# Kernel optimization log

Measured on AMD Instinct MI355X. Metric: run time of the kernel, lower is better.

Reference implementation:

```python
import jax, jax.numpy as jnp
import numpy as np

B, C_IN, H, W = 8, 64, 128, 128
NUM_POINT = 128
N_INST = 512
INIT_STRIDE, COARSE_STRIDE, DOWN_SAMPLE = 10.0, 4.0, 4.0
D_MODEL, N_HEADS = 256, 8


def conv2d(x, w, b, pad):
    y = jax.lax.conv_general_dilated(x, w, (1, 1), [(pad, pad), (pad, pad)],
                                     dimension_numbers=('NCHW', 'OIHW', 'NCHW'))
    return y + b[None, :, None, None]


def trans_feature(x, w1, b1, w2, b2):
    # Conv3x3 -> ReLU -> Conv1x1 (c_in -> 256 -> 254)
    return conv2d(jax.nn.relu(conv2d(x, w1, b1, 1)), w2, b2, 0)


def grid_sample_points(feat, img_idx, pts):
    # get_gcn_feature: per-instance bilinear sampling of feat[img_idx] at pixel
    # coords pts. torch grid_sample(align_corners=False, padding_mode='zeros');
    # the normalize->unnormalize of pixel coords collapses to a -0.5 shift.
    Bf, C, Hf, Wf = feat.shape
    ix = pts[..., 0] - 0.5
    iy = pts[..., 1] - 0.5
    x0 = jnp.floor(ix)
    y0 = jnp.floor(iy)
    wx = ix - x0
    wy = iy - y0

    def gather(yy, xx, wgt):
        valid = (xx >= 0) & (xx < Wf) & (yy >= 0) & (yy < Hf)
        xc = jnp.clip(xx, 0, Wf - 1).astype(jnp.int32)
        yc = jnp.clip(yy, 0, Hf - 1).astype(jnp.int32)
        v = feat[img_idx[:, None], :, yc, xc]  # [N,P,C]
        return v * (wgt * valid)[..., None]

    return (gather(y0, x0, (1 - wx) * (1 - wy)) + gather(y0, x0 + 1, wx * (1 - wy))
            + gather(y0 + 1, x0, (1 - wx) * wy) + gather(y0 + 1, x0 + 1, wx * wy))


def normalize_poly(poly):
    # Center each contour and scale by its max extent -> positional encoding in [-1,1]
    mean = poly.mean(axis=1, keepdims=True)
    p = poly - mean
    scale = jnp.max(jnp.abs(p), axis=(1, 2), keepdims=True) + 1e-6
    return p / scale


def csa(x, wqkv, bqkv, wo, bo, whead, bhead):
    # ContourSelfAttention: MHSA over contour points + linear head to 2D offsets
    N, P, C = x.shape
    d = C // N_HEADS
    qkv = x @ wqkv + bqkv
    q, k, v = jnp.split(qkv, 3, axis=-1)
    sh = lambda t: t.reshape(N, P, N_HEADS, d).transpose(0, 2, 1, 3)
    q, k, v = sh(q), sh(k), sh(v)
    attn = jax.nn.softmax(jnp.einsum('nhpd,nhqd->nhpq', q, k) / jnp.sqrt(jnp.float32(d)), axis=-1)
    o = jnp.einsum('nhpq,nhqd->nhpd', attn, v).transpose(0, 2, 1, 3).reshape(N, P, C)
    o = o @ wo + bo
    return o @ whead + bhead  # [N,P,2]


def setup_inputs():
    key = jax.random.key(0)
    ks = jax.random.split(key, 32)
    s = 0.05
    inp = {
        'cnn_feature': jax.random.normal(ks[0], (B, C_IN, H, W), jnp.float32),
        'wh_pred': jax.random.normal(ks[1], (B, 2 * NUM_POINT, H, W), jnp.float32),
        'ct_ind': jax.random.randint(ks[2], (N_INST,), 0, H * W),
        'ct_img_idx': jax.random.randint(ks[3], (N_INST,), 0, B),
    }
    p = lambda i, shape: jax.random.normal(ks[i], shape, jnp.float32) * s
    for pre, i0 in (('f1', 4), ('f2', 8)):
        inp[pre + '_w1'] = p(i0, (256, C_IN, 3, 3))
        inp[pre + '_b1'] = p(i0 + 1, (256,))
        inp[pre + '_w2'] = p(i0 + 2, (254, 256, 1, 1))
        inp[pre + '_b2'] = p(i0 + 3, (254,))
    for pre, i0 in (('csa1', 12), ('csa2', 18)):
        inp[pre + '_wqkv'] = p(i0, (D_MODEL, 3 * D_MODEL))
        inp[pre + '_bqkv'] = p(i0 + 1, (3 * D_MODEL,))
        inp[pre + '_wo'] = p(i0 + 2, (D_MODEL, D_MODEL))
        inp[pre + '_bo'] = p(i0 + 3, (D_MODEL,))
        inp[pre + '_whead'] = p(i0 + 4, (D_MODEL, 2))
        inp[pre + '_bhead'] = p(i0 + 5, (2,))
    return inp


def reference(cnn_feature, wh_pred, ct_ind, ct_img_idx,
              f1_w1, f1_b1, f1_w2, f1_b2, f2_w1, f2_b1, f2_w2, f2_b2,
              csa1_wqkv, csa1_bqkv, csa1_wo, csa1_bo, csa1_whead, csa1_bhead,
              csa2_wqkv, csa2_bqkv, csa2_wo, csa2_bo, csa2_whead, csa2_bhead):
    # ---- Decode.train_decode ----
    ct_x = ct_ind % W
    ct_y = ct_ind // W
    # per-instance gather of contour offsets: wh_pred[img, :, y, x] -> [N, 2*P]
    ct_offset = wh_pred[ct_img_idx, :, ct_y, ct_x].reshape(-1, NUM_POINT, 2)
    ct = jnp.stack([ct_x, ct_y], axis=1).astype(jnp.float32)  # [N,2]
    init_polys = ct_offset * INIT_STRIDE + ct[:, None, :]     # [N,128,2]
    # ---- Refine ----
    feat1 = trans_feature(cnn_feature, f1_w1, f1_b1, f1_w2, f1_b2)  # [B,254,H,W]
    feat2 = trans_feature(cnn_feature, f2_w1, f2_b1, f2_w2, f2_b2)
    points = jnp.concatenate([ct[:, None, :], init_polys], axis=1)  # [N,129,2]
    fp1 = grid_sample_points(feat1, ct_img_idx, points)             # [N,129,254]
    x1 = jnp.concatenate([fp1, normalize_poly(points)], axis=-1)    # [N,129,256]
    offsets1 = csa(x1, csa1_wqkv, csa1_bqkv, csa1_wo, csa1_bo, csa1_whead, csa1_bhead)[:, 1:, :]
    coarse_polys = offsets1 * COARSE_STRIDE + jax.lax.stop_gradient(init_polys)
    fp2 = grid_sample_points(feat2, ct_img_idx, coarse_polys)       # [N,128,254]
    x2 = jnp.concatenate([fp2, normalize_poly(coarse_polys)], axis=-1)
    offsets2 = csa(x2, csa2_wqkv, csa2_bqkv, csa2_wo, csa2_bo, csa2_whead, csa2_bhead)
    final_polys = offsets2 + jax.lax.stop_gradient(coarse_polys)
    return (init_polys * DOWN_SAMPLE, coarse_polys * DOWN_SAMPLE, final_polys * DOWN_SAMPLE)
```

## Files before the change

kernel.cpp:

```cpp
#include <hip/hip_runtime.h>
#include <hip/hip_bf16.h>

typedef unsigned short u16;
typedef unsigned int   u32;
typedef float  f32x4 __attribute__((ext_vector_type(4)));
typedef short  s16x8 __attribute__((ext_vector_type(8)));

__device__ __forceinline__ float bf2f(u16 u) {
    return __uint_as_float(((unsigned int)u) << 16);
}
__device__ __forceinline__ u16 f2bf(float f) {
    unsigned int x = __float_as_uint(f);
    unsigned int r = x + 0x7fffu + ((x >> 16) & 1u);
    return (u16)(r >> 16);
}

#define WIMG 128
#define HIMG 128
#define PADW 130
#define BIMG 8
#define CIN  64
#define NPOINT 128
#define NINST 512

#define AS1 __attribute__((address_space(1)))
#define AS3 __attribute__((address_space(3)))
__device__ __forceinline__ void async16(const void* g, void* l) {
    __builtin_amdgcn_global_load_lds((const AS1 void*)g, (AS3 void*)l, 16, 0, 0);
}

__global__ __launch_bounds__(256) void k_cvt_w1(const float* __restrict__ w,
                                                u16* __restrict__ wb) {
    int idx = blockIdx.x * 256 + threadIdx.x;
    int oc = idx / 576, r = idx % 576;
    int kp = r >> 6, ic = r & 63;
    wb[idx] = f2bf(w[oc * 576 + ic * 9 + kp]);
}

__global__ __launch_bounds__(256) void k_cvt_w2(const float* __restrict__ w,
                                                u16* __restrict__ wb) {
    int idx = blockIdx.x * 256 + threadIdx.x;
    int oc = idx >> 8, ic = idx & 255;
    wb[idx] = (oc < 254) ? f2bf(w[oc * 256 + ic]) : (u16)0;
}

__global__ __launch_bounds__(256) void k_cvt_wqkv(const float* __restrict__ w,
                                                  u16* __restrict__ wb) {
    int idx = blockIdx.x * 256 + threadIdx.x;
    int n = idx >> 8, k = idx & 255;
    wb[idx] = f2bf(w[k * 768 + n]);
}

__global__ __launch_bounds__(256) void k_headfuse(const float* __restrict__ wo,
                                                  const float* __restrict__ bo,
                                                  const float* __restrict__ whead,
                                                  const float* __restrict__ bhead,
                                                  float* __restrict__ W2,
                                                  float* __restrict__ b2) {
    int idx = blockIdx.x * 256 + threadIdx.x;
    if (idx < 512) {
        int c = idx >> 1, j = idx & 1;
        float s = 0.f;
        for (int t = 0; t < 256; ++t)
            s = fmaf(wo[c * 256 + t], whead[t * 2 + j], s);
        W2[idx] = s;
    }
    if (idx < 2) {
        float s = bhead[idx];
        for (int t = 0; t < 256; ++t)
            s = fmaf(bo[t], whead[t * 2 + idx], s);
        b2[idx] = s;
    }
}

__global__ __launch_bounds__(256) void k_zero(u16* __restrict__ p) {
    int i = blockIdx.x * 256 + threadIdx.x;
    ((uint4*)p)[i] = make_uint4(0u, 0u, 0u, 0u);
}

__global__ __launch_bounds__(256) void k_nhwc(const float* __restrict__ in,
                                              u16* __restrict__ out) {
    __shared__ u16 sT[128][80];
    int b = blockIdx.x >> 7, y = blockIdx.x & 127;
    int tid = threadIdx.x;
    const float* ib = in + ((size_t)b * CIN * HIMG + y) * WIMG;
    int x4 = tid & 31, icg = tid >> 5;
    #pragma unroll
    for (int pass = 0; pass < 8; ++pass) {
        int ic = pass * 8 + icg;
        float4 v = *(const float4*)&ib[(size_t)ic * (HIMG * WIMG) + x4 * 4];
        sT[x4 * 4 + 0][ic] = f2bf(v.x);
        sT[x4 * 4 + 1][ic] = f2bf(v.y);
        sT[x4 * 4 + 2][ic] = f2bf(v.z);
        sT[x4 * 4 + 3][ic] = f2bf(v.w);
    }
    __syncthreads();
    u16* ob = out + ((size_t)(b * PADW + y + 1) * PADW + 1) * 64;
    int icu = tid & 7, xw = tid >> 3;
    #pragma unroll
    for (int pass = 0; pass < 4; ++pass) {
        int x = pass * 32 + xw;
        uint4 v = *(const uint4*)&sT[x][icu * 8];
        *(uint4*)&ob[(size_t)x * 64 + icu * 8] = v;
    }
}

__global__ __launch_bounds__(256) void k_init(const float* __restrict__ whp,
                                              const int* __restrict__ ct_ind,
                                              const int* __restrict__ ct_img,
                                              float* __restrict__ points1,
                                              float* __restrict__ out0) {
    int i = blockIdx.x;
    int t = threadIdx.x;
    int ind = ct_ind[i];
    int x = ind % WIMG, y = ind / WIMG;
    int b = ct_img[i];
    int p = t >> 1, c = t & 1;
    float off = whp[(((size_t)b * 2 * NPOINT + t) * HIMG + y) * WIMG + x];
    float ctc = (c == 0) ? (float)x : (float)y;
    float ip = off * 10.0f + ctc;
    points1[((size_t)i * 129 + 1 + p) * 2 + c] = ip;
    if (t < 2) points1[(size_t)i * 129 * 2 + t] = (t == 0) ? (float)x : (float)y;
    out0[((size_t)i * NPOINT + p) * 2 + c] = ip * 4.0f;
}

__global__ __launch_bounds__(256, 2) void k_convgemm(const u16* __restrict__ inTp,
                                                     const u16* __restrict__ wb1,
                                                     const float* __restrict__ b1,
                                                     const u16* __restrict__ wb2,
                                                     const float* __restrict__ b2,
                                                     u16* __restrict__ feat) {
    __shared__ u16 smem[33280];
    u16* sB = smem;
    u16* sW = smem + 16384;
    u16* sC = smem + 16384;

    int tid = threadIdx.x;
    int wave = tid >> 6, lane = tid & 63;
    int quad = lane >> 4, l16 = lane & 15;
    int rl = lane >> 2, part = lane & 3;
    int partS = part ^ ((rl ^ (rl >> 2)) & 3);
    int quadS = quad ^ ((l16 ^ (l16 >> 2)) & 3);

    int bx = blockIdx.x;
    int y = (bx & 7) * 16 + (bx >> 4);
    int half = (bx >> 3) & 1;
    int xb = half * 64;
    int b = blockIdx.z;
    const u16* inb = inTp + (size_t)b * PADW * PADW * 64;

    for (int idx = tid; idx < 1584; idx += 256) {
        int r = idx / 528, g = idx - r * 528;
        int pxw = g >> 3, c = g & 7;
        uint4 v = *(const uint4*)&inb[((size_t)(y + r) * PADW + xb + pxw) * 64 + c * 8];
        *(uint4*)&sW[((r * 66 + pxw) * 8 + (c ^ (pxw & 7))) * 8] = v;
    }

    auto stageB1 = [&](u16* dst, int t) {
        int kp = t >> 1, ic0 = (t & 1) << 5;
        const u16* brow = wb1 + (size_t)kp * 64 + ic0 + partS * 8;
        #pragma unroll
        for (int j = 0; j < 4; ++j) {
            int rr = wave * 64 + j * 16;
            async16(brow + (size_t)(rr + rl) * 576, dst + rr * 32);
        }
    };
    auto stageB2 = [&](u16* dst, int kk) {
        #pragma unroll
        for (int j = 0; j < 4; ++j) {
            int rr = wave * 64 + j * 16;
            async16(wb2 + (size_t)(rr + rl) * 256 + kk + partS * 8, dst + rr * 32);
        }
    };

    f32x4 acc1[4][4];
    #pragma unroll
    for (int mt = 0; mt < 4; ++mt)
        #pragma unroll
        for (int nt = 0; nt < 4; ++nt)
            #pragma unroll
            for (int q = 0; q < 4; ++q) acc1[mt][nt][q] = 0.f;

    stageB1(sB, 0);
    __syncthreads();
    int buf = 0;
    for (int t = 0; t < 18; ++t) {
        if (t < 17) stageB1(sB + (buf ^ 1) * 8192, t + 1);
        int kp = t >> 1, cdb = (t & 1) << 2;
        int ky = kp / 3, kx = kp - ky * 3;
        s16x8 aF[4], bF[4];
        #pragma unroll
        for (int mt = 0; mt < 4; ++mt) {
            int pxw = kx + mt * 16 + l16;
            int cd = cdb + quad;
            aF[mt] = *(const s16x8*)&sW[((ky * 66 + pxw) * 8 + (cd ^ (pxw & 7))) * 8];
        }
        #pragma unroll
        for (int nt = 0; nt < 4; ++nt)
            bF[nt] = *(const s16x8*)&sB[buf * 8192 + (wave * 64 + nt * 16 + l16) * 32 + quadS * 8];
        #pragma unroll
        for (int mt = 0; mt < 4; ++mt)
            #pragma unroll
            for (int nt = 0; nt < 4; ++nt)
                acc1[mt][nt] = __builtin_amdgcn_mfma_f32_16x16x32_bf16(
                    aF[mt], bF[nt], acc1[mt][nt], 0, 0, 0);
        __syncthreads();
        buf ^= 1;
    }

    #pragma unroll
    for (int nt = 0; nt < 4; ++nt) {
        int col = wave * 64 + nt * 16 + l16;
        float bv = b1[col];
        #pragma unroll
        for (int mt = 0; mt < 4; ++mt) {
            #pragma unroll
            for (int r = 0; r < 4; ++r) {
                int row = mt * 16 + quad * 4 + r;
                sC[row * 264 + col] = f2bf(fmaxf(acc1[mt][nt][r] + bv, 0.f));
            }
        }
    }
    stageB2(sB, 0);
    __syncthreads();

    f32x4 acc2[4][4];
    #pragma unroll
    for (int mt = 0; mt < 4; ++mt)
        #pragma unroll
        for (int nt = 0; nt < 4; ++nt)
            #pragma unroll
            for (int q = 0; q < 4; ++q) acc2[mt][nt][q] = 0.f;
    int b2f = 0;
    for (int ik = 0; ik < 8; ++ik) {
        if (ik < 7) stageB2(sB + (b2f ^ 1) * 8192, (ik + 1) * 32);
        s16x8 a2[4], bb[4];
        #pragma unroll
        for (int mt = 0; mt < 4; ++mt)
            a2[mt] = *(const s16x8*)&sC[(mt * 16 + l16) * 264 + ik * 32 + quad * 8];
        #pragma unroll
        for (int nt = 0; nt < 4; ++nt)
            bb[nt] = *(const s16x8*)&sB[b2f * 8192 + (wave * 64 + nt * 16 + l16) * 32 + quadS * 8];
        #pragma unroll
        for (int mt = 0; mt < 4; ++mt)
            #pragma unroll
            for (int nt = 0; nt < 4; ++nt)
                acc2[mt][nt] = __builtin_amdgcn_mfma_f32_16x16x32_bf16(
                    a2[mt], bb[nt], acc2[mt][nt], 0, 0, 0);
        __syncthreads();
        b2f ^= 1;
    }

    #pragma unroll
    for (int nt = 0; nt < 4; ++nt) {
        int col = wave * 64 + nt * 16 + l16;
        float bv = (col < 254) ? b2[col] : 0.f;
        #pragma unroll
        for (int mt = 0; mt < 4; ++mt) {
            #pragma unroll
            for (int r = 0; r < 4; ++r) {
                int row = mt * 16 + quad * 4 + r;
                sC[row * 264 + col] = f2bf(acc2[mt][nt][r] + bv);
            }
        }
    }
    __syncthreads();
    u16* outb = feat + ((size_t)b * (HIMG * WIMG) + (size_t)y * 128 + half * 64) * 256;
    #pragma unroll
    for (int it = 0; it < 8; ++it) {
        int idx = it * 256 + tid;
        int row = idx >> 5, ch = idx & 31;
        *(uint4*)&outb[(size_t)row * 256 + ch * 8] = *(const uint4*)&sC[row * 264 + ch * 8];
    }
}

__global__ __launch_bounds__(256, 4) void k_gemm_mfma(const u16* __restrict__ A,
                                                      const u16* __restrict__ Bt,
                                                      const float* __restrict__ bias, int nbias,
                                                      u16* __restrict__ C,
                                                      int M, int N, int K, int relu) {
    __shared__ u16 smem[16384];
    u16* sA = smem;
    u16* sB = smem + 8192;
    u16* sOut = smem;
    int tid = threadIdx.x;
    int wave = tid >> 6, lane = tid & 63;
    int quad = lane >> 4, l16 = lane & 15;
    int rl = lane >> 2, part = lane & 3;
    int partS = part ^ ((rl ^ (rl >> 2)) & 3);
    int quadS = quad ^ ((l16 ^ (l16 >> 2)) & 3);
    int r0 = wave * 32;

    int gx = gridDim.x, gy = gridDim.y;
    int o = blockIdx.y * gx + blockIdx.x;
    int nwg = gx * gy;
    int qn = nwg >> 3, r8 = nwg & 7;
    int xcd = o & 7, oi = o >> 3;
    int vid = (xcd < r8) ? xcd * (qn + 1) + oi : r8 * (qn + 1) + (xcd - r8) * qn + oi;
    int m0 = (vid / gy) * 128, n0 = (vid % gy) * 128;
    int wm = (wave >> 1) * 64, wn = (wave & 1) * 64;

    f32x4 acc[4][4];
    #pragma unroll
    for (int a = 0; a < 4; ++a)
        #pragma unroll
        for (int b = 0; b < 4; ++b)
            #pragma unroll
            for (int q = 0; q < 4; ++q) acc[a][b][q] = 0.f;

    auto stage = [&](int bufi, int kk) {
        #pragma unroll
        for (int j = 0; j < 2; ++j) {
            int rr = r0 + j * 16;
            async16(&A[(size_t)(m0 + rr + rl) * K + kk + partS * 8], &sA[bufi * 4096 + rr * 32]);
            async16(&Bt[(size_t)(n0 + rr + rl) * K + kk + partS * 8], &sB[bufi * 4096 + rr * 32]);
        }
    };

    stage(0, 0);
    __syncthreads();
    int buf = 0;
    int nk = K >> 5;
    for (int ik = 0; ik < nk; ++ik) {
        if (ik + 1 < nk) stage(buf ^ 1, (ik + 1) << 5);
        s16x8 aF[4], bF[4];
        #pragma unroll
        for (int mt = 0; mt < 4; ++mt)
            aF[mt] = *(const s16x8*)&sA[buf * 4096 + (wm + mt * 16 + l16) * 32 + quadS * 8];
        #pragma unroll
        for (int nt = 0; nt < 4; ++nt)
            bF[nt] = *(const s16x8*)&sB[buf * 4096 + (wn + nt * 16 + l16) * 32 + quadS * 8];
        #pragma unroll
        for (int mt = 0; mt < 4; ++mt)
            #pragma unroll
            for (int nt = 0; nt < 4; ++nt)
                acc[mt][nt] = __builtin_amdgcn_mfma_f32_16x16x32_bf16(
                    aF[mt], bF[nt], acc[mt][nt], 0, 0, 0);
        __syncthreads();
        buf ^= 1;
    }

    #pragma unroll
    for (int pass = 0; pass < 2; ++pass) {
        if ((wave >> 1) == pass) {
            #pragma unroll
            for (int nt = 0; nt < 4; ++nt) {
                int col = wn + nt * 16 + l16;
                int gcol = n0 + col;
                float bv = (gcol < nbias) ? bias[gcol] : 0.f;
                #pragma unroll
                for (int mt = 0; mt < 4; ++mt) {
                    #pragma unroll
                    for (int r = 0; r < 4; ++r) {
                        int rowl = mt * 16 + quad * 4 + r;
                        float v = acc[mt][nt][r] + bv;
                        if (relu) v = fmaxf(v, 0.f);
                        sOut[rowl * 132 + col] = f2bf(v);
                    }
                }
            }
        }
        __syncthreads();
        #pragma unroll
        for (int it = 0; it < 8; ++it) {
            int idx = it * 256 + tid;
            int rowl = idx >> 5, ch = idx & 31;
            *(uint2*)&C[(size_t)(m0 + pass * 64 + rowl) * N + n0 + ch * 4] =
                *(const uint2*)&sOut[rowl * 132 + ch * 4];
        }
        __syncthreads();
    }
}

__global__ __launch_bounds__(256) void k_norm(const float* __restrict__ pts,
                                              u16* __restrict__ xout, int P) {
    int i = blockIdx.x, t = threadIdx.x;
    __shared__ float sx[256], sy[256];
    float px = 0.f, py = 0.f;
    if (t < P) {
        px = pts[((size_t)i * P + t) * 2 + 0];
        py = pts[((size_t)i * P + t) * 2 + 1];
    }
    sx[t] = px; sy[t] = py;
    __syncthreads();
    for (int s = 128; s > 0; s >>= 1) {
        if (t < s) { sx[t] += sx[t + s]; sy[t] += sy[t + s]; }
        __syncthreads();
    }
    float mx = sx[0] / (float)P, my = sy[0] / (float)P;
    __syncthreads();
    float ax = 0.f;
    if (t < P) ax = fmaxf(fabsf(px - mx), fabsf(py - my));
    sx[t] = ax;
    __syncthreads();
    for (int s = 128; s > 0; s >>= 1) {
        if (t < s) sx[t] = fmaxf(sx[t], sx[t + s]);
        __syncthreads();
    }
    float scale = sx[0] + 1e-6f;
    if (t < P) {
        size_t base = ((size_t)i * P + t) * 256;
        xout[base + 254] = f2bf((px - mx) / scale);
        xout[base + 255] = f2bf((py - my) / scale);
    }
}

__global__ __launch_bounds__(256) void k_sample(const u16* __restrict__ feat,
                                                const float* __restrict__ pts,
                                                const int* __restrict__ ct_img,
                                                u16* __restrict__ xout, int P) {
    int i = blockIdx.x;
    int p = blockIdx.y * 2 + (threadIdx.x >> 7);
    int c0 = (threadIdx.x & 127) * 2;
    if (p >= P || c0 >= 254) return;
    float px = pts[((size_t)i * P + p) * 2 + 0];
    float py = pts[((size_t)i * P + p) * 2 + 1];
    int b = ct_img[i];
    float ix = px - 0.5f, iy = py - 0.5f;
    float x0f = floorf(ix), y0f = floorf(iy);
    float wx = ix - x0f, wy = iy - y0f;
    int x0 = (int)x0f, y0 = (int)y0f;
    float a0 = 0.f, a1 = 0.f;
    #pragma unroll
    for (int dy = 0; dy < 2; ++dy) {
        #pragma unroll
        for (int dx = 0; dx < 2; ++dx) {
            int xx = x0 + dx, yy = y0 + dy;
            float w = (dx ? wx : 1.f - wx) * (dy ? wy : 1.f - wy);
            if (xx >= 0 && xx < WIMG && yy >= 0 && yy < HIMG) {
                u32 v = *(const u32*)&feat[(((size_t)b * HIMG + yy) * WIMG + xx) * 256 + c0];
                a0 = fmaf(w, bf2f((u16)(v & 0xffffu)), a0);
                a1 = fmaf(w, bf2f((u16)(v >> 16)), a1);
            }
        }
    }
    u32 st = (u32)f2bf(a0) | ((u32)f2bf(a1) << 16);
    *(u32*)&xout[((size_t)i * P + p) * 256 + c0] = st;
}

__global__ __launch_bounds__(256) void k_attn_mfma(const u16* __restrict__ qkv,
                                                   u16* __restrict__ obuf,
                                                   int P) {
    __shared__ u16 smem[144 * 40 * 2 + 32 * 168];
    u16* sQ = smem;
    u16* sK = smem + 144 * 40;
    u16* sVT = smem + 2 * 144 * 40;

    int il = blockIdx.x, h = blockIdx.y;
    int tid = threadIdx.x;
    int wave = tid >> 6, lane = tid & 63;
    int quad = lane >> 4, l16 = lane & 15;

    {
        u32* z = (u32*)smem;
        for (int i = tid; i < (144 * 40 * 2 + 32 * 168) / 2; i += 256) z[i] = 0u;
    }
    __syncthreads();
    for (int idx = tid; idx < 129 * 16 && (idx >> 4) < P; idx += 256) {
        int row = idx >> 4, c2 = idx & 15;
        size_t gb = ((size_t)il * P + row) * 768 + h * 32 + c2 * 2;
        *(u32*)&sQ[row * 40 + c2 * 2] = *(const u32*)&qkv[gb];
        *(u32*)&sK[row * 40 + c2 * 2] = *(const u32*)&qkv[gb + 256];
        u32 v = *(const u32*)&qkv[gb + 512];
        int kin = row & 31;
        int pcol = (row & ~31) + ((kin >> 2) & 3) * 8 + (kin >> 4) * 4 + (kin & 3);
        int d0 = c2 * 2;
        sVT[d0 * 168 + pcol] = (u16)(v & 0xffffu);
        sVT[(d0 + 1) * 168 + pcol] = (u16)(v >> 16);
    }
    __syncthreads();

    const float scale = 0.17677669529663689f;
    for (int qt = wave; qt < 9; qt += 4) {
        s16x8 bq = *(const s16x8*)&sQ[(qt * 16 + l16) * 40 + quad * 8];
        f32x4 s4[9];
        #pragma unroll
        for (int kt = 0; kt < 9; ++kt) {
            s16x8 aK = *(const s16x8*)&sK[(kt * 16 + l16) * 40 + quad * 8];
            f32x4 zz = {0.f, 0.f, 0.f, 0.f};
            s4[kt] = __builtin_amdgcn_mfma_f32_16x16x32_bf16(aK, bq, zz, 0, 0, 0);
        }
        float mx = -1e30f;
        #pragma unroll
        for (int kt = 0; kt < 9; ++kt)
            #pragma unroll
            for (int r = 0; r < 4; ++r) {
                int k = kt * 16 + quad * 4 + r;
                float v = (k < P) ? s4[kt][r] * scale : -1e30f;
                s4[kt][r] = v;
                mx = fmaxf(mx, v);
            }
        mx = fmaxf(mx, __shfl_xor(mx, 16));
        mx = fmaxf(mx, __shfl_xor(mx, 32));
        float l = 0.f;
        #pragma unroll
        for (int kt = 0; kt < 9; ++kt)
            #pragma unroll
            for (int r = 0; r < 4; ++r) {
                float e = __expf(s4[kt][r] - mx);
                s4[kt][r] = e;
                l += e;
            }
        l += __shfl_xor(l, 16);
        l += __shfl_xor(l, 32);
        u16 pb[9][4];
        #pragma unroll
        for (int kt = 0; kt < 9; ++kt)
            #pragma unroll
            for (int r = 0; r < 4; ++r) pb[kt][r] = f2bf(s4[kt][r]);
        f32x4 o[2];
        #pragma unroll
        for (int mt = 0; mt < 2; ++mt)
            #pragma unroll
            for (int q = 0; q < 4; ++q) o[mt][q] = 0.f;
        #pragma unroll
        for (int t = 0; t < 5; ++t) {
            s16x8 bp;
            #pragma unroll
            for (int j = 0; j < 4; ++j) bp[j] = (short)pb[2 * t][j];
            #pragma unroll
            for (int j = 0; j < 4; ++j)
                bp[4 + j] = (2 * t + 1 < 9) ? (short)pb[2 * t + 1][j] : (short)0;
            #pragma unroll
            for (int mt = 0; mt < 2; ++mt) {
                s16x8 aV = *(const s16x8*)&sVT[(mt * 16 + l16) * 168 + t * 32 + quad * 8];
                o[mt] = __builtin_amdgcn_mfma_f32_16x16x32_bf16(aV, bp, o[mt], 0, 0, 0);
            }
        }
        int q = qt * 16 + l16;
        if (q < P) {
            float inv = 1.f / l;
            size_t ob = ((size_t)il * P + q) * 256 + h * 32;
            #pragma unroll
            for (int mt = 0; mt < 2; ++mt) {
                ushort4 st;
                st.x = f2bf(o[mt][0] * inv);
                st.y = f2bf(o[mt][1] * inv);
                st.z = f2bf(o[mt][2] * inv);
                st.w = f2bf(o[mt][3] * inv);
                *(ushort4*)&obuf[ob + mt * 16 + quad * 4] = st;
            }
        }
    }
}

__global__ __launch_bounds__(256) void k_head1(const u16* __restrict__ obuf,
                                               const float* __restrict__ W2,
                                               const float* __restrict__ b2,
                                               const float* __restrict__ pts1,
                                               float* __restrict__ coarse,
                                               float* __restrict__ out1) {
    int wave = threadIdx.x >> 6, lane = threadIdx.x & 63;
    int m = blockIdx.x * 4 + wave;
    const u16* orow = obuf + (size_t)m * 256;
    ushort4 u = *(const ushort4*)(orow + lane * 4);
    float4 w0 = *(const float4*)(W2 + lane * 8);
    float4 w1 = *(const float4*)(W2 + lane * 8 + 4);
    float c0 = bf2f(u.x), c1 = bf2f(u.y), c2 = bf2f(u.z), c3 = bf2f(u.w);
    float s0 = c0 * w0.x + c1 * w0.z + c2 * w1.x + c3 * w1.z;
    float s1 = c0 * w0.y + c1 * w0.w + c2 * w1.y + c3 * w1.w;
    for (int off = 32; off > 0; off >>= 1) {
        s0 += __shfl_down(s0, off);
        s1 += __shfl_down(s1, off);
    }
    if (lane == 0) {
        int i = m / 129, p = m % 129;
        if (p > 0) {
            float o0 = s0 + b2[0], o1 = s1 + b2[1];
            float i0 = pts1[(size_t)m * 2 + 0];
            float i1 = pts1[(size_t)m * 2 + 1];
            float cc0 = o0 * 4.f + i0, cc1 = o1 * 4.f + i1;
            size_t cm = (size_t)i * 128 + (p - 1);
            coarse[cm * 2 + 0] = cc0;
            coarse[cm * 2 + 1] = cc1;
            out1[cm * 2 + 0] = cc0 * 4.f;
            out1[cm * 2 + 1] = cc1 * 4.f;
        }
    }
}

__global__ __launch_bounds__(256) void k_head2(const u16* __restrict__ obuf,
                                               const float* __restrict__ W2,
                                               const float* __restrict__ b2,
                                               const float* __restrict__ coarse,
                                               float* __restrict__ out2) {
    int wave = threadIdx.x >> 6, lane = threadIdx.x & 63;
    int m = blockIdx.x * 4 + wave;
    const u16* orow = obuf + (size_t)m * 256;
    ushort4 u = *(const ushort4*)(orow + lane * 4);
    float4 w0 = *(const float4*)(W2 + lane * 8);
    float4 w1 = *(const float4*)(W2 + lane * 8 + 4);
    float c0 = bf2f(u.x), c1 = bf2f(u.y), c2 = bf2f(u.z), c3 = bf2f(u.w);
    float s0 = c0 * w0.x + c1 * w0.z + c2 * w1.x + c3 * w1.z;
    float s1 = c0 * w0.y + c1 * w0.w + c2 * w1.y + c3 * w1.w;
    for (int off = 32; off > 0; off >>= 1) {
        s0 += __shfl_down(s0, off);
        s1 += __shfl_down(s1, off);
    }
    if (lane == 0) {
        float f0 = s0 + b2[0] + coarse[(size_t)m * 2 + 0];
        float f1 = s1 + b2[1] + coarse[(size_t)m * 2 + 1];
        out2[(size_t)m * 2 + 0] = f0 * 4.f;
        out2[(size_t)m * 2 + 1] = f1 * 4.f;
    }
}

extern "C" void kernel_launch(void* const* d_in, const int* in_sizes, int n_in,
                              void* d_out, int out_size, void* d_ws, size_t ws_size,
                              hipStream_t stream) {
    const float* cnn     = (const float*)d_in[0];
    const float* whp     = (const float*)d_in[1];
    const int*   ct_ind  = (const int*)d_in[2];
    const int*   ct_img  = (const int*)d_in[3];
    const float* f1_w1   = (const float*)d_in[4];
    const float* f1_b1   = (const float*)d_in[5];
    const float* f1_w2   = (const float*)d_in[6];
    const float* f1_b2   = (const float*)d_in[7];
    const float* f2_w1   = (const float*)d_in[8];
    const float* f2_b1   = (const float*)d_in[9];
    const float* f2_w2   = (const float*)d_in[10];
    const float* f2_b2   = (const float*)d_in[11];
    const float* c1_wqkv = (const float*)d_in[12];
    const float* c1_bqkv = (const float*)d_in[13];
    const float* c1_wo   = (const float*)d_in[14];
    const float* c1_bo   = (const float*)d_in[15];
    const float* c1_wh   = (const float*)d_in[16];
    const float* c1_bh   = (const float*)d_in[17];
    const float* c2_wqkv = (const float*)d_in[18];
    const float* c2_bqkv = (const float*)d_in[19];
    const float* c2_wo   = (const float*)d_in[20];
    const float* c2_bo   = (const float*)d_in[21];
    const float* c2_wh   = (const float*)d_in[22];
    const float* c2_bh   = (const float*)d_in[23];

    char* ws = (char*)d_ws;
    float* points1 = (float*)(ws + 0);
    float* coarse  = (float*)(ws + 528384);
    float* W2_1    = (float*)(ws + 1052672);
    float* b2_1    = (float*)(ws + 1054720);
    float* W2_2    = (float*)(ws + 1054976);
    float* b2_2    = (float*)(ws + 1057024);
    u16*   wb1a    = (u16*)(ws + 1057280);
    u16*   wb1b    = (u16*)(ws + 1352192);
    u16*   wb2a    = (u16*)(ws + 1647104);
    u16*   wb2b    = (u16*)(ws + 1778176);
    u16*   wqT1    = (u16*)(ws + 1909248);
    u16*   wqT2    = (u16*)(ws + 2302464);
    u16*   inT     = (u16*)(ws + 2695680);
    u16*   feat    = (u16*)(ws + 20001280);
    u16*   xbuf    = (u16*)(ws + 87110144);
    u16*   qkv_all = (u16*)(ws + 120926720);

    float* out0 = (float*)d_out;
    float* out1 = out0 + 131072;
    float* out2 = out0 + 262144;

    k_cvt_w1<<<576, 256, 0, stream>>>(f1_w1, wb1a);
    k_cvt_w1<<<576, 256, 0, stream>>>(f2_w1, wb1b);
    k_cvt_w2<<<256, 256, 0, stream>>>(f1_w2, wb2a);
    k_cvt_w2<<<256, 256, 0, stream>>>(f2_w2, wb2b);
    k_cvt_wqkv<<<768, 256, 0, stream>>>(c1_wqkv, wqT1);
    k_cvt_wqkv<<<768, 256, 0, stream>>>(c2_wqkv, wqT2);
    k_headfuse<<<2, 256, 0, stream>>>(c1_wo, c1_bo, c1_wh, c1_bh, W2_1, b2_1);
    k_headfuse<<<2, 256, 0, stream>>>(c2_wo, c2_bo, c2_wh, c2_bh, W2_2, b2_2);
    k_init<<<NINST, 256, 0, stream>>>(whp, ct_ind, ct_img, points1, out0);
    k_zero<<<4225, 256, 0, stream>>>(inT);
    k_nhwc<<<1024, 256, 0, stream>>>(cnn, inT);

    k_convgemm<<<dim3(256, 1, 8), 256, 0, stream>>>(inT, wb1a, f1_b1, wb2a, f1_b2, feat);
    k_norm<<<NINST, 256, 0, stream>>>(points1, xbuf, 129);
    k_sample<<<dim3(NINST, 65), 256, 0, stream>>>(feat, points1, ct_img, xbuf, 129);
    k_gemm_mfma<<<dim3(516, 6), 256, 0, stream>>>(xbuf, wqT1, c1_bqkv, 768, qkv_all,
                                                  66048, 768, 256, 0);
    k_attn_mfma<<<dim3(NINST, 8), 256, 0, stream>>>(qkv_all, xbuf, 129);
    k_head1<<<16512, 256, 0, stream>>>(xbuf, W2_1, b2_1, points1, coarse, out1);

    k_convgemm<<<dim3(256, 1, 8), 256, 0, stream>>>(inT, wb1b, f2_b1, wb2b, f2_b2, feat);
    k_norm<<<NINST, 256, 0, stream>>>(coarse, xbuf, 128);
    k_sample<<<dim3(NINST, 64), 256, 0, stream>>>(feat, coarse, ct_img, xbuf, 128);
    k_gemm_mfma<<<dim3(512, 6), 256, 0, stream>>>(xbuf, wqT2, c2_bqkv, 768, qkv_all,
                                                  65536, 768, 256, 0);
    k_attn_mfma<<<dim3(NINST, 8), 256, 0, stream>>>(qkv_all, xbuf, 128);
    k_head2<<<16384, 256, 0, stream>>>(xbuf, W2_2, b2_2, coarse, out2);
}
```

Measured before the change: 755.5 us.

## Prefetch two stages ahead with explicit vmcnt waits and zero only halo

The conv-GEMM and the QKV GEMM main loops now issue global-to-LDS loads two K-steps ahead. They use manual s_waitcnt vmcnt and raw s_barrier with scheduling barriers in place of __syncthreads, so loads overlap more compute and a full wait is no longer forced each iteration. The padded NHWC input buffer is no longer fully zeroed; only the one-pixel halo border is cleared, since the interior is overwritten by the transpose kernel. The hand-tuned vmcnt counts depend on the exact number of outstanding async loads per thread, so a miscount could introduce races.

```diff
diff --git a/kernel.cpp b/kernel.cpp
--- a/kernel.cpp
+++ b/kernel.cpp
@@ -28,6 +28,12 @@
 __device__ __forceinline__ void async16(const void* g, void* l) {
     __builtin_amdgcn_global_load_lds((const AS1 void*)g, (AS3 void*)l, 16, 0, 0);
 }
+
+#define SWAIT_VM4()   asm volatile("s_waitcnt vmcnt(4)" ::: "memory")
+#define SWAIT_VM0()   asm volatile("s_waitcnt vmcnt(0)" ::: "memory")
+#define SWAIT_LGKM0() asm volatile("s_waitcnt lgkmcnt(0)" ::: "memory")
+#define SBAR()        __builtin_amdgcn_s_barrier()
+#define SCHED0()      __builtin_amdgcn_sched_barrier(0)
 
 __global__ __launch_bounds__(256) void k_cvt_w1(const float* __restrict__ w,
                                                 u16* __restrict__ wb) {
@@ -73,9 +79,18 @@
     }
 }
 
-__global__ __launch_bounds__(256) void k_zero(u16* __restrict__ p) {
-    int i = blockIdx.x * 256 + threadIdx.x;
-    ((uint4*)p)[i] = make_uint4(0u, 0u, 0u, 0u);
+__global__ __launch_bounds__(256) void k_halo(u16* __restrict__ p) {
+    int idx = blockIdx.x * 256 + threadIdx.x;
+    if (idx >= 33024) return;
+    int img = idx / 4128, r = idx % 4128;
+    int h = r >> 3, c = r & 7;
+    int x, y;
+    if (h < 130)      { y = 0;   x = h; }
+    else if (h < 260) { y = 129; x = h - 130; }
+    else if (h < 388) { x = 0;   y = h - 259; }
+    else              { x = 129; y = h - 387; }
+    *(uint4*)&p[(((size_t)img * PADW + y) * PADW + x) * 64 + c * 8] =
+        make_uint4(0u, 0u, 0u, 0u);
 }
 
 __global__ __launch_bounds__(256) void k_nhwc(const float* __restrict__ in,
@@ -181,11 +196,7 @@
             #pragma unroll
             for (int q = 0; q < 4; ++q) acc1[mt][nt][q] = 0.f;
 
-    stageB1(sB, 0);
-    __syncthreads();
-    int buf = 0;
-    for (int t = 0; t < 18; ++t) {
-        if (t < 17) stageB1(sB + (buf ^ 1) * 8192, t + 1);
+    auto body1 = [&](int buf, int t) {
         int kp = t >> 1, cdb = (t & 1) << 2;
         int ky = kp / 3, kx = kp - ky * 3;
         s16x8 aF[4], bF[4];
@@ -204,8 +215,17 @@
             for (int nt = 0; nt < 4; ++nt)
                 acc1[mt][nt] = __builtin_amdgcn_mfma_f32_16x16x32_bf16(
                     aF[mt], bF[nt], acc1[mt][nt], 0, 0, 0);
-        __syncthreads();
-        buf ^= 1;
+    };
+
+    stageB1(sB, 0);
+    stageB1(sB + 8192, 1);
+    SWAIT_LGKM0();
+    for (int t = 0; t < 18; ++t) {
+        if (t < 17) { SWAIT_VM4(); } else { SWAIT_VM0(); }
+        SBAR(); SCHED0();
+        body1(t & 1, t);
+        SCHED0(); SBAR();
+        if (t < 16) stageB1(sB + (t & 1) * 8192, t + 2);
     }
 
     #pragma unroll
@@ -221,8 +241,6 @@
             }
         }
     }
-    stageB2(sB, 0);
-    __syncthreads();
 
     f32x4 acc2[4][4];
     #pragma unroll
@@ -231,24 +249,32 @@
         for (int nt = 0; nt < 4; ++nt)
             #pragma unroll
             for (int q = 0; q < 4; ++q) acc2[mt][nt][q] = 0.f;
-    int b2f = 0;
-    for (int ik = 0; ik < 8; ++ik) {
-        if (ik < 7) stageB2(sB + (b2f ^ 1) * 8192, (ik + 1) * 32);
+
+    auto body2 = [&](int buf, int ik) {
         s16x8 a2[4], bb[4];
         #pragma unroll
         for (int mt = 0; mt < 4; ++mt)
             a2[mt] = *(const s16x8*)&sC[(mt * 16 + l16) * 264 + ik * 32 + quad * 8];
         #pragma unroll
         for (int nt = 0; nt < 4; ++nt)
-            bb[nt] = *(const s16x8*)&sB[b2f * 8192 + (wave * 64 + nt * 16 + l16) * 32 + quadS * 8];
+            bb[nt] = *(const s16x8*)&sB[buf * 8192 + (wave * 64 + nt * 16 + l16) * 32 + quadS * 8];
         #pragma unroll
         for (int mt = 0; mt < 4; ++mt)
             #pragma unroll
             for (int nt = 0; nt < 4; ++nt)
                 acc2[mt][nt] = __builtin_amdgcn_mfma_f32_16x16x32_bf16(
                     a2[mt], bb[nt], acc2[mt][nt], 0, 0, 0);
-        __syncthreads();
-        b2f ^= 1;
+    };
+
+    stageB2(sB, 0);
+    stageB2(sB + 8192, 32);
+    SWAIT_LGKM0();
+    for (int ik = 0; ik < 8; ++ik) {
+        if (ik < 7) { SWAIT_VM4(); } else { SWAIT_VM0(); }
+        SBAR(); SCHED0();
+        body2(ik & 1, ik);
+        SCHED0(); SBAR();
+        if (ik < 6) stageB2(sB + (ik & 1) * 8192, (ik + 2) * 32);
     }
 
     #pragma unroll
@@ -316,13 +342,7 @@
             async16(&Bt[(size_t)(n0 + rr + rl) * K + kk + partS * 8], &sB[bufi * 4096 + rr * 32]);
         }
     };
-
-    stage(0, 0);
-    __syncthreads();
-    int buf = 0;
-    int nk = K >> 5;
-    for (int ik = 0; ik < nk; ++ik) {
-        if (ik + 1 < nk) stage(buf ^ 1, (ik + 1) << 5);
+    auto body = [&](int buf) {
         s16x8 aF[4], bF[4];
         #pragma unroll
         for (int mt = 0; mt < 4; ++mt)
@@ -336,8 +356,17 @@
             for (int nt = 0; nt < 4; ++nt)
                 acc[mt][nt] = __builtin_amdgcn_mfma_f32_16x16x32_bf16(
                     aF[mt], bF[nt], acc[mt][nt], 0, 0, 0);
-        __syncthreads();
-        buf ^= 1;
+    };
+
+    int nk = K >> 5;
+    stage(0, 0);
+    stage(1, 32);
+    for (int ik = 0; ik < nk; ++ik) {
+        if (ik < nk - 1) { SWAIT_VM4(); } else { SWAIT_VM0(); }
+        SBAR(); SCHED0();
+        body(ik & 1);
+        SCHED0(); SBAR();
+        if (ik + 2 < nk) stage(ik & 1, (ik + 2) << 5);
     }
 
     #pragma unroll
@@ -664,7 +693,7 @@
     k_headfuse<<<2, 256, 0, stream>>>(c1_wo, c1_bo, c1_wh, c1_bh, W2_1, b2_1);
     k_headfuse<<<2, 256, 0, stream>>>(c2_wo, c2_bo, c2_wh, c2_bh, W2_2, b2_2);
     k_init<<<NINST, 256, 0, stream>>>(whp, ct_ind, ct_img, points1, out0);
-    k_zero<<<4225, 256, 0, stream>>>(inT);
+    k_halo<<<130, 256, 0, stream>>>(inT);
     k_nhwc<<<1024, 256, 0, stream>>>(cnn, inT);
 
     k_convgemm<<<dim3(256, 1, 8), 256, 0, stream>>>(inT, wb1a, f1_b1, wb2a, f1_b2, feat);
```

After: 763.6 us. Within noise of the previous version (+1.1%).
